# Kernel optimization log

Hardware: AMD Instinct MI355X
Metric: run time of the kernel (lower is better)

The kernel has to match this reference:

```python
import jax, jax.numpy as jnp
import numpy as np

EPS = 1e-6


def setup_inputs() -> dict:
    key = jax.random.key(0)
    k1, k2, k3, k4 = jax.random.split(key, 4)
    B, N, D = 8, 4096, 512
    x = jax.random.normal(k1, (B, N, D), dtype=jnp.float32)
    # torch nn.Linear(dim, 3*dim, bias=False): weight shape [3D, D], y = x @ W.T
    w_qkv = jax.random.normal(k2, (3 * D, D), dtype=jnp.float32) * (1.0 / np.sqrt(D))
    w_proj = jax.random.normal(k3, (D, D), dtype=jnp.float32) * (1.0 / np.sqrt(D))
    b_proj = jax.random.normal(k4, (D,), dtype=jnp.float32) * 0.01
    return {"x": x, "w_qkv": w_qkv, "w_proj": w_proj, "b_proj": b_proj, "heads": 8}


def reference(x, w_qkv, w_proj, b_proj, heads):
    B, N, D = x.shape
    H = heads
    d = D // H
    # qkv projection -> (3, B, H, N, d)
    qkv = (x @ w_qkv.T).reshape(B, N, 3, H, d).transpose(2, 0, 3, 1, 4)
    q, k, v = qkv[0], qkv[1], qkv[2]
    # elu+1 feature map (positive features)
    q = jax.nn.elu(q) + 1.0 + EPS
    k = jax.nn.elu(k) + 1.0 + EPS
    # kv summary: [B,H,d,d]
    kv = jnp.einsum('bhnd,bhne->bhde', k, v)
    # denominator: q . sum_n(k) -> [B,H,N]
    denom = jnp.einsum('bhnd,bhd->bhn', q, k.sum(axis=2))
    out = jnp.einsum('bhnd,bhde->bhne', q, kv) / (denom[..., None] + EPS)
    out = out.transpose(0, 2, 1, 3).reshape(B, N, D)
    return out @ w_proj.T + b_proj
```

## Files before the change

### kernel.cpp

```cpp
#include <hip/hip_runtime.h>
#include <hip/hip_bf16.h>
#include <math.h>

#define EPSF 1e-6f

constexpr int Bc = 8;
constexpr int Nc = 4096;
constexpr int Dc = 512;
constexpr int QKVC = 3 * Dc;

typedef __attribute__((ext_vector_type(8))) short short8v;
typedef __attribute__((ext_vector_type(8))) unsigned short ushort8v;
typedef __attribute__((ext_vector_type(4))) float float4v;

__device__ __forceinline__ unsigned short f2bf(float f) {
    union { float f; unsigned int u; } v; v.f = f;
    unsigned int u = v.u;
    return (unsigned short)((u + 0x7fffu + ((u >> 16) & 1u)) >> 16);
}
__device__ __forceinline__ float bf2f(unsigned short h) {
    union { unsigned int u; float f; } v; v.u = ((unsigned int)h) << 16;
    return v.f;
}

typedef __attribute__((address_space(1))) const void gvoid_t;
typedef __attribute__((address_space(3))) void lvoid_t;
__device__ __forceinline__ void llds16(const void* g, void* l) {
    __builtin_amdgcn_global_load_lds((gvoid_t*)g, (lvoid_t*)l, 16, 0, 0);
}

__global__ __launch_bounds__(256) void cvt_f32_bf16(
    const float* __restrict__ in, unsigned short* __restrict__ out, int n8)
{
    int i = blockIdx.x * 256 + threadIdx.x;
    if (i >= n8) return;
    float4 a = reinterpret_cast<const float4*>(in)[2 * i];
    float4 b = reinterpret_cast<const float4*>(in)[2 * i + 1];
    ushort8v o;
    o[0] = f2bf(a.x); o[1] = f2bf(a.y); o[2] = f2bf(a.z); o[3] = f2bf(a.w);
    o[4] = f2bf(b.x); o[5] = f2bf(b.y); o[6] = f2bf(b.z); o[7] = f2bf(b.w);
    reinterpret_cast<ushort8v*>(out)[i] = o;
}

__global__ __launch_bounds__(512, 2) void gemm_qkv(
    const unsigned short* __restrict__ A,
    const unsigned short* __restrict__ Bm,
    unsigned short* __restrict__ Cout)
{
    constexpr int LDA = 512, LDB = 512, LDC = 1536;
    constexpr int NT = 8;
    __shared__ unsigned short ring[3][24576];

    const int t = threadIdx.x;
    const int orig = blockIdx.x;
    const int wg = (orig & 7) * 192 + (orig >> 3);
    const int bm = (wg / 12) * 256;
    const int bn = (wg % 12) * 128;

    const int w = t >> 6, lane = t & 63;
    const int ln = lane & 15, g = lane >> 4;
    const int wr = (w >> 1) * 64;
    const int wc = (w & 1) * 64;
    const int l7 = ln & 7;

    const int rs = t >> 3;
    const int ci = t & 7;
    const int swz = ci ^ (rs & 7);
    const unsigned short* As0 = A + (size_t)(bm + rs) * LDA + swz * 8;
    const unsigned short* As1 = A + (size_t)(bm + 64 + rs) * LDA + swz * 8;
    const unsigned short* As2 = A + (size_t)(bm + 128 + rs) * LDA + swz * 8;
    const unsigned short* As3 = A + (size_t)(bm + 192 + rs) * LDA + swz * 8;
    const unsigned short* Bs0 = Bm + (size_t)(bn + rs) * LDB + swz * 8;
    const unsigned short* Bs1 = Bm + (size_t)(bn + 64 + rs) * LDB + swz * 8;

#define STAGEQ(Tt) do {                                                        \
        const int k0_ = (Tt) * 64;                                             \
        unsigned short* dA_ = &ring[(Tt) % 3][0];                              \
        unsigned short* dB_ = &ring[(Tt) % 3][16384];                          \
        llds16(As0 + k0_, dA_ + (size_t)t * 8);                                \
        llds16(As1 + k0_, dA_ + (size_t)(512 + t) * 8);                        \
        llds16(As2 + k0_, dA_ + (size_t)(1024 + t) * 8);                       \
        llds16(As3 + k0_, dA_ + (size_t)(1536 + t) * 8);                       \
        llds16(Bs0 + k0_, dB_ + (size_t)t * 8);                                \
        llds16(Bs1 + k0_, dB_ + (size_t)(512 + t) * 8);                        \
    } while (0)

    float4v acc[4][4];
#pragma unroll
    for (int i = 0; i < 4; ++i)
#pragma unroll
        for (int j = 0; j < 4; ++j) acc[i][j] = {0.f, 0.f, 0.f, 0.f};

    STAGEQ(0);
    STAGEQ(1);
    asm volatile("s_waitcnt vmcnt(6)" ::: "memory");
    __builtin_amdgcn_s_barrier();
    __builtin_amdgcn_sched_barrier(0);

#pragma unroll
    for (int T = 0; T < NT; ++T) {
        if (T + 2 < NT) STAGEQ(T + 2);

        const unsigned short* base = &ring[T % 3][0];
        short8v a[4][2], b[4][2];
#pragma unroll
        for (int i = 0; i < 4; ++i)
#pragma unroll
            for (int kk = 0; kk < 2; ++kk) {
                const int row = wr + i * 16 + ln;
                a[i][kk] = *reinterpret_cast<const short8v*>(
                    base + row * 64 + (((kk * 4 + g) ^ l7) << 3));
            }
#pragma unroll
        for (int j = 0; j < 4; ++j)
#pragma unroll
            for (int kk = 0; kk < 2; ++kk) {
                const int row = wc + j * 16 + ln;
                b[j][kk] = *reinterpret_cast<const short8v*>(
                    base + 16384 + row * 64 + (((kk * 4 + g) ^ l7) << 3));
            }

        __builtin_amdgcn_s_setprio(1);
#pragma unroll
        for (int kk = 0; kk < 2; ++kk)
#pragma unroll
            for (int i = 0; i < 4; ++i)
#pragma unroll
                for (int j = 0; j < 4; ++j)
                    acc[i][j] = __builtin_amdgcn_mfma_f32_16x16x32_bf16(
                        a[i][kk], b[j][kk], acc[i][j], 0, 0, 0);
        __builtin_amdgcn_s_setprio(0);

        if (T + 1 < NT) {
            if (T + 2 < NT)
                asm volatile("s_waitcnt vmcnt(6)" ::: "memory");
            else
                asm volatile("s_waitcnt vmcnt(0)" ::: "memory");
            __builtin_amdgcn_s_barrier();
            __builtin_amdgcn_sched_barrier(0);
        }
    }
#undef STAGEQ

#pragma unroll
    for (int i = 0; i < 4; ++i) {
        const int Rb = bm + wr + i * 16 + g * 4;
#pragma unroll
        for (int j = 0; j < 4; ++j) {
            const int Cc = bn + wc + j * 16 + ln;
            const bool do_elu = (Cc < 1024);
#pragma unroll
            for (int r = 0; r < 4; ++r) {
                float v = acc[i][j][r];
                if (do_elu) v = (v > 0.f) ? (v + 1.0f + EPSF) : (expf(v) + EPSF);
                Cout[(size_t)(Rb + r) * LDC + Cc] = f2bf(v);
            }
        }
    }
}

__global__ __launch_bounds__(256) void kv_part(
    const unsigned short* __restrict__ qkv,
    float* __restrict__ kvp, float* __restrict__ ksp)
{
    const int bh = blockIdx.x, chunk = blockIdx.y;
    const int b = bh >> 3, h = bh & 7;

    __shared__ float kt[64][68];
    __shared__ float vt[64][68];
    __shared__ float ksl[4][64];

    const int t  = threadIdx.x;
    const int e  = t & 63, dg = t >> 6;
    const int rr = t >> 3, slot = t & 7;

    float acc[16] = {};
    float ks = 0.f;

    const size_t base = ((size_t)b * Nc + (size_t)chunk * 512) * QKVC + h * 64;

    for (int n0 = 0; n0 < 512; n0 += 64) {
#pragma unroll
        for (int half = 0; half < 2; ++half) {
            const int row = rr + half * 32;
            const unsigned short* kr = qkv + base + (size_t)(n0 + row) * QKVC + Dc + slot * 8;
            const unsigned short* vr = kr + Dc;
            ushort8v kq = *reinterpret_cast<const ushort8v*>(kr);
            ushort8v vq = *reinterpret_cast<const ushort8v*>(vr);
            float4 k0 = make_float4(bf2f(kq[0]), bf2f(kq[1]), bf2f(kq[2]), bf2f(kq[3]));
            float4 k1 = make_float4(bf2f(kq[4]), bf2f(kq[5]), bf2f(kq[6]), bf2f(kq[7]));
            float4 v0 = make_float4(bf2f(vq[0]), bf2f(vq[1]), bf2f(vq[2]), bf2f(vq[3]));
            float4 v1 = make_float4(bf2f(vq[4]), bf2f(vq[5]), bf2f(vq[6]), bf2f(vq[7]));
            *reinterpret_cast<float4*>(&kt[row][slot * 8])     = k0;
            *reinterpret_cast<float4*>(&kt[row][slot * 8 + 4]) = k1;
            *reinterpret_cast<float4*>(&vt[row][slot * 8])     = v0;
            *reinterpret_cast<float4*>(&vt[row][slot * 8 + 4]) = v1;
        }
        __syncthreads();
#pragma unroll 2
        for (int nn = 0; nn < 64; ++nn) {
            const float vv = vt[nn][e];
            const float4 q0 = *reinterpret_cast<const float4*>(&kt[nn][dg * 16]);
            const float4 q1 = *reinterpret_cast<const float4*>(&kt[nn][dg * 16 + 4]);
            const float4 q2 = *reinterpret_cast<const float4*>(&kt[nn][dg * 16 + 8]);
            const float4 q3 = *reinterpret_cast<const float4*>(&kt[nn][dg * 16 + 12]);
            acc[0]  += q0.x * vv; acc[1]  += q0.y * vv; acc[2]  += q0.z * vv; acc[3]  += q0.w * vv;
            acc[4]  += q1.x * vv; acc[5]  += q1.y * vv; acc[6]  += q1.z * vv; acc[7]  += q1.w * vv;
            acc[8]  += q2.x * vv; acc[9]  += q2.y * vv; acc[10] += q2.z * vv; acc[11] += q2.w * vv;
            acc[12] += q3.x * vv; acc[13] += q3.y * vv; acc[14] += q3.z * vv; acc[15] += q3.w * vv;
        }
#pragma unroll
        for (int nn = 0; nn < 16; ++nn) ks += kt[dg * 16 + nn][e];
        __syncthreads();
    }

    float* kvpp = kvp + ((size_t)bh * 8 + chunk) * 4096;
#pragma unroll
    for (int i = 0; i < 16; ++i) kvpp[(dg * 16 + i) * 64 + e] = acc[i];

    ksl[dg][e] = ks;
    __syncthreads();
    if (t < 64) ksp[((size_t)bh * 8 + chunk) * 64 + t] =
        ksl[0][t] + ksl[1][t] + ksl[2][t] + ksl[3][t];
}

__global__ __launch_bounds__(256) void kv_reduce(
    const float* __restrict__ kvp, const float* __restrict__ ksp,
    unsigned short* __restrict__ kvT, float* __restrict__ ksum)
{
    const int bh = blockIdx.x, t = threadIdx.x;
    const float* src = kvp + (size_t)bh * 8 * 4096;
#pragma unroll
    for (int i = 0; i < 16; ++i) {
        const int idx = i * 256 + t;
        float s = 0.f;
#pragma unroll
        for (int c = 0; c < 8; ++c) s += src[c * 4096 + idx];
        const int d = idx >> 6, e = idx & 63;
        kvT[(size_t)bh * 4096 + e * 64 + d] = f2bf(s);
    }
    if (t < 64) {
        float s = 0.f;
#pragma unroll
        for (int c = 0; c < 8; ++c) s += ksp[((size_t)bh * 8 + c) * 64 + t];
        ksum[bh * 64 + t] = s;
    }
}

__global__ __launch_bounds__(256) void attn_proj(
    const unsigned short* __restrict__ qkv,
    const unsigned short* __restrict__ kvT,
    const float* __restrict__ ksum,
    const unsigned short* __restrict__ wp,
    const float* __restrict__ bias,
    float* __restrict__ out)
{
    __shared__ unsigned short lq[128 * 64];
    __shared__ unsigned short lkv[64 * 64];
    __shared__ unsigned short lwp[128 * 64];
    __shared__ unsigned short loL[128 * 64];

    const int t = threadIdx.x;
    const int rowBlk = blockIdx.x;
    const int bn = blockIdx.y;
    const int b = rowBlk >> 5;
    const size_t rowBase = (size_t)rowBlk * 128;

    const int w = t >> 6, lane = t & 63;
    const int ln = lane & 15, g = lane >> 4;
    const int wr = (w >> 1) * 64, wc = (w & 1) * 64;
    const int l7 = ln & 7;

    char* lqc  = (char*)lq;
    char* lkvc = (char*)lkv;
    char* lwpc = (char*)lwp;
    char* loLc = (char*)loL;

    float4v accP[4][4];
#pragma unroll
    for (int i = 0; i < 4; ++i)
#pragma unroll
        for (int j = 0; j < 4; ++j) accP[i][j] = {0.f, 0.f, 0.f, 0.f};

    for (int h = 0; h < 8; ++h) {
        const int bh = b * 8 + h;
        const unsigned short* qsrc = qkv + rowBase * QKVC + h * 64;
        const unsigned short* wsrc = wp + (size_t)(bn * 128) * 512 + h * 64;
        const unsigned short* ksrc = kvT + (size_t)bh * 4096;

#pragma unroll
        for (int s = 0; s < 4; ++s) {
            const int c = s * 256 + t, r = c >> 3, ci = c & 7;
            ushort8v qv = *reinterpret_cast<const ushort8v*>(qsrc + (size_t)r * QKVC + ci * 8);
            *reinterpret_cast<ushort8v*>(lqc + r * 128 + ((ci ^ (r & 7)) << 4)) = qv;
            ushort8v wv = *reinterpret_cast<const ushort8v*>(wsrc + (size_t)r * 512 + ci * 8);
            *reinterpret_cast<ushort8v*>(lwpc + r * 128 + ((ci ^ (r & 7)) << 4)) = wv;
        }
#pragma unroll
        for (int s = 0; s < 2; ++s) {
            const int c = s * 256 + t, r = c >> 3, ci = c & 7;
            ushort8v kvv = *reinterpret_cast<const ushort8v*>(ksrc + r * 64 + ci * 8);
            *reinterpret_cast<ushort8v*>(lkvc + r * 128 + ((ci ^ (r & 7)) << 4)) = kvv;
        }
        __syncthreads();

        float ksv[2][8];
        {
            const float* ksb = ksum + bh * 64 + g * 8;
            float4 a0 = *reinterpret_cast<const float4*>(ksb);
            float4 a1 = *reinterpret_cast<const float4*>(ksb + 4);
            float4 b0 = *reinterpret_cast<const float4*>(ksb + 32);
            float4 b1 = *reinterpret_cast<const float4*>(ksb + 36);
            ksv[0][0] = a0.x; ksv[0][1] = a0.y; ksv[0][2] = a0.z; ksv[0][3] = a0.w;
            ksv[0][4] = a1.x; ksv[0][5] = a1.y; ksv[0][6] = a1.z; ksv[0][7] = a1.w;
            ksv[1][0] = b0.x; ksv[1][1] = b0.y; ksv[1][2] = b0.z; ksv[1][3] = b0.w;
            ksv[1][4] = b1.x; ksv[1][5] = b1.y; ksv[1][6] = b1.z; ksv[1][7] = b1.w;
        }

        short8v akv[4][2], bq[2][2];
#pragma unroll
        for (int i = 0; i < 4; ++i)
#pragma unroll
            for (int kk = 0; kk < 2; ++kk)
                akv[i][kk] = *reinterpret_cast<const short8v*>(
                    lkvc + (i * 16 + ln) * 128 + (((kk * 4 + g) ^ l7) << 4));
#pragma unroll
        for (int j = 0; j < 2; ++j)
#pragma unroll
            for (int kk = 0; kk < 2; ++kk)
                bq[j][kk] = *reinterpret_cast<const short8v*>(
                    lqc + (w * 32 + j * 16 + ln) * 128 + (((kk * 4 + g) ^ l7) << 4));

        float4v acco[4][2];
#pragma unroll
        for (int i = 0; i < 4; ++i)
#pragma unroll
            for (int j = 0; j < 2; ++j) acco[i][j] = {0.f, 0.f, 0.f, 0.f};
#pragma unroll
        for (int kk = 0; kk < 2; ++kk)
#pragma unroll
            for (int i = 0; i < 4; ++i)
#pragma unroll
                for (int j = 0; j < 2; ++j)
                    acco[i][j] = __builtin_amdgcn_mfma_f32_16x16x32_bf16(
                        akv[i][kk], bq[j][kk], acco[i][j], 0, 0, 0);

        float inv[2];
#pragma unroll
        for (int j = 0; j < 2; ++j) {
            float p = 0.f;
#pragma unroll
            for (int kk = 0; kk < 2; ++kk)
#pragma unroll
                for (int m = 0; m < 8; ++m)
                    p += bf2f((unsigned short)bq[j][kk][m]) * ksv[kk][m];
            p += __shfl_xor(p, 16);
            p += __shfl_xor(p, 32);
            inv[j] = 1.0f / (p + EPSF);
        }

#pragma unroll
        for (int i = 0; i < 4; ++i)
#pragma unroll
            for (int j = 0; j < 2; ++j) {
                unsigned int p0 = (unsigned int)f2bf(acco[i][j][0] * inv[j]) |
                                  ((unsigned int)f2bf(acco[i][j][1] * inv[j]) << 16);
                unsigned int p1 = (unsigned int)f2bf(acco[i][j][2] * inv[j]) |
                                  ((unsigned int)f2bf(acco[i][j][3] * inv[j]) << 16);
                const int row = w * 32 + j * 16 + ln;
                const int chunk = i * 2 + (g >> 1);
                char* dst = loLc + row * 128 + (((chunk ^ l7) << 4) | ((g & 1) << 3));
                *reinterpret_cast<uint2*>(dst) = make_uint2(p0, p1);
            }
        __syncthreads();

        short8v ao[4][2], bw[4][2];
#pragma unroll
        for (int i = 0; i < 4; ++i)
#pragma unroll
            for (int kk = 0; kk < 2; ++kk)
                ao[i][kk] = *reinterpret_cast<const short8v*>(
                    loLc + (wr + i * 16 + ln) * 128 + (((kk * 4 + g) ^ l7) << 4));
#pragma unroll
        for (int j = 0; j < 4; ++j)
#pragma unroll
            for (int kk = 0; kk < 2; ++kk)
                bw[j][kk] = *reinterpret_cast<const short8v*>(
                    lwpc + (wc + j * 16 + ln) * 128 + (((kk * 4 + g) ^ l7) << 4));

        __builtin_amdgcn_s_setprio(1);
#pragma unroll
        for (int kk = 0; kk < 2; ++kk)
#pragma unroll
            for (int i = 0; i < 4; ++i)
#pragma unroll
                for (int j = 0; j < 4; ++j)
                    accP[i][j] = __builtin_amdgcn_mfma_f32_16x16x32_bf16(
                        ao[i][kk], bw[j][kk], accP[i][j], 0, 0, 0);
        __builtin_amdgcn_s_setprio(0);
        __syncthreads();
    }

#pragma unroll
    for (int j = 0; j < 4; ++j) {
        const int col = bn * 128 + wc + j * 16 + ln;
        const float bv = bias[col];
#pragma unroll
        for (int i = 0; i < 4; ++i) {
            const size_t rg = rowBase + wr + i * 16 + g * 4;
#pragma unroll
            for (int rr = 0; rr < 4; ++rr)
                out[(rg + rr) * 512 + col] = accP[i][j][rr] + bv;
        }
    }
}

extern "C" void kernel_launch(void* const* d_in, const int* in_sizes, int n_in,
                              void* d_out, int out_size, void* d_ws, size_t ws_size,
                              hipStream_t stream)
{
    const float* x      = (const float*)d_in[0];
    const float* w_qkv  = (const float*)d_in[1];
    const float* w_proj = (const float*)d_in[2];
    const float* b_proj = (const float*)d_in[3];
    float* out = (float*)d_out;

    char* ws = (char*)d_ws;
    unsigned short* qkvb = (unsigned short*)ws;
    size_t off = (size_t)32768 * 1536 * 2;
    unsigned short* xb   = (unsigned short*)(ws + off); off += (size_t)32768 * 512 * 2;
    unsigned short* wqb  = (unsigned short*)(ws + off); off += (size_t)1536 * 512 * 2;
    unsigned short* wpb  = (unsigned short*)(ws + off); off += (size_t)512 * 512 * 2;
    float* kvp           = (float*)(ws + off);          off += (size_t)64 * 8 * 4096 * 4;
    float* ksp           = (float*)(ws + off);          off += (size_t)64 * 8 * 64 * 4;
    unsigned short* kvT  = (unsigned short*)(ws + off); off += (size_t)64 * 4096 * 2;
    float* ksumb         = (float*)(ws + off);

    cvt_f32_bf16<<<dim3((32768 * 512 / 8 + 255) / 256), dim3(256), 0, stream>>>(x, xb, 32768 * 512 / 8);
    cvt_f32_bf16<<<dim3((1536 * 512 / 8 + 255) / 256), dim3(256), 0, stream>>>(w_qkv, wqb, 1536 * 512 / 8);
    cvt_f32_bf16<<<dim3((512 * 512 / 8 + 255) / 256), dim3(256), 0, stream>>>(w_proj, wpb, 512 * 512 / 8);

    gemm_qkv<<<dim3(1536), dim3(512), 0, stream>>>(xb, wqb, qkvb);

    kv_part<<<dim3(64, 8), dim3(256), 0, stream>>>(qkvb, kvp, ksp);
    kv_reduce<<<dim3(64), dim3(256), 0, stream>>>(kvp, ksp, kvT, ksumb);

    attn_proj<<<dim3(256, 4), dim3(256), 0, stream>>>(
        qkvb, kvT, ksumb, wpb, b_proj, out);
}
```

Before: 195.2 us.

## Use 256x256 QKV GEMM tiles with double buffering and interleaved phased staging

The QKV GEMM tile grows from 256x128 to 256x256, halving the grid to 768 blocks, and each wave now covers a 128x64 sub-tile. The 3-stage LDS ring becomes a double buffer, with loads for the next k-tile split into four chunks that are issued between barrier-separated MFMA phases. The aim is more data reuse per LDS byte and global loads that overlap compute in a ping-pong schedule. In exchange it uses 64KB of LDS and twice the accumulator registers, which may lower occupancy below the 2 blocks requested, and it adds more barriers per k-step.

Measured after the change: 203.3 us. 4.2% more time.

```diff
diff --git a/kernel.cpp b/kernel.cpp
--- a/kernel.cpp
+++ b/kernel.cpp
@@ -49,109 +49,130 @@
 {
     constexpr int LDA = 512, LDB = 512, LDC = 1536;
     constexpr int NT = 8;
-    __shared__ unsigned short ring[3][24576];
+    __shared__ unsigned short lA[2][16384];
+    __shared__ unsigned short lB[2][16384];
 
     const int t = threadIdx.x;
     const int orig = blockIdx.x;
-    const int wg = (orig & 7) * 192 + (orig >> 3);
-    const int bm = (wg / 12) * 256;
-    const int bn = (wg % 12) * 128;
+    const int wg = (orig & 7) * 96 + (orig >> 3);
+    const int bm = (wg / 6) * 256;
+    const int bn = (wg % 6) * 256;
 
     const int w = t >> 6, lane = t & 63;
     const int ln = lane & 15, g = lane >> 4;
-    const int wr = (w >> 1) * 64;
-    const int wc = (w & 1) * 64;
+    const int wm = (w >> 2) * 128;
+    const int wn = (w & 3) * 64;
     const int l7 = ln & 7;
 
-    const int rs = t >> 3;
-    const int ci = t & 7;
+    const int rs = t >> 3, ci = t & 7;
     const int swz = ci ^ (rs & 7);
-    const unsigned short* As0 = A + (size_t)(bm + rs) * LDA + swz * 8;
-    const unsigned short* As1 = A + (size_t)(bm + 64 + rs) * LDA + swz * 8;
-    const unsigned short* As2 = A + (size_t)(bm + 128 + rs) * LDA + swz * 8;
-    const unsigned short* As3 = A + (size_t)(bm + 192 + rs) * LDA + swz * 8;
-    const unsigned short* Bs0 = Bm + (size_t)(bn + rs) * LDB + swz * 8;
-    const unsigned short* Bs1 = Bm + (size_t)(bn + 64 + rs) * LDB + swz * 8;
-
-#define STAGEQ(Tt) do {                                                        \
-        const int k0_ = (Tt) * 64;                                             \
-        unsigned short* dA_ = &ring[(Tt) % 3][0];                              \
-        unsigned short* dB_ = &ring[(Tt) % 3][16384];                          \
-        llds16(As0 + k0_, dA_ + (size_t)t * 8);                                \
-        llds16(As1 + k0_, dA_ + (size_t)(512 + t) * 8);                        \
-        llds16(As2 + k0_, dA_ + (size_t)(1024 + t) * 8);                       \
-        llds16(As3 + k0_, dA_ + (size_t)(1536 + t) * 8);                       \
-        llds16(Bs0 + k0_, dB_ + (size_t)t * 8);                                \
-        llds16(Bs1 + k0_, dB_ + (size_t)(512 + t) * 8);                        \
-    } while (0)
-
-    float4v acc[4][4];
-#pragma unroll
-    for (int i = 0; i < 4; ++i)
+    const unsigned short* Ab = A + (size_t)(bm + rs) * LDA + swz * 8;
+    const unsigned short* Bb = Bm + (size_t)(bn + rs) * LDB + swz * 8;
+
+#define STG_A(Tt, r4) llds16(Ab + (size_t)(r4) * 64 * LDA + (Tt) * 64, \
+                             &lA[(Tt) & 1][((r4) * 512 + t) * 8])
+#define STG_B(Tt, r4) llds16(Bb + (size_t)(r4) * 64 * LDB + (Tt) * 64, \
+                             &lB[(Tt) & 1][((r4) * 512 + t) * 8])
+#define PH_BAR() do { __builtin_amdgcn_s_barrier(); \
+                      __builtin_amdgcn_sched_barrier(0); } while (0)
+
+    float4v acc[8][4];
+#pragma unroll
+    for (int i = 0; i < 8; ++i)
 #pragma unroll
         for (int j = 0; j < 4; ++j) acc[i][j] = {0.f, 0.f, 0.f, 0.f};
 
-    STAGEQ(0);
-    STAGEQ(1);
-    asm volatile("s_waitcnt vmcnt(6)" ::: "memory");
-    __builtin_amdgcn_s_barrier();
-    __builtin_amdgcn_sched_barrier(0);
+    STG_A(0, 0); STG_A(0, 1); STG_A(0, 2); STG_A(0, 3);
+    STG_B(0, 0); STG_B(0, 1); STG_B(0, 2); STG_B(0, 3);
+    asm volatile("s_waitcnt vmcnt(0)" ::: "memory");
+    PH_BAR();
 
 #pragma unroll
     for (int T = 0; T < NT; ++T) {
-        if (T + 2 < NT) STAGEQ(T + 2);
-
-        const unsigned short* base = &ring[T % 3][0];
-        short8v a[4][2], b[4][2];
-#pragma unroll
-        for (int i = 0; i < 4; ++i)
-#pragma unroll
-            for (int kk = 0; kk < 2; ++kk) {
-                const int row = wr + i * 16 + ln;
-                a[i][kk] = *reinterpret_cast<const short8v*>(
-                    base + row * 64 + (((kk * 4 + g) ^ l7) << 3));
-            }
-#pragma unroll
-        for (int j = 0; j < 4; ++j)
-#pragma unroll
-            for (int kk = 0; kk < 2; ++kk) {
-                const int row = wc + j * 16 + ln;
-                b[j][kk] = *reinterpret_cast<const short8v*>(
-                    base + 16384 + row * 64 + (((kk * 4 + g) ^ l7) << 3));
-            }
-
+        const unsigned short* pa = lA[T & 1];
+        const unsigned short* pb = lB[T & 1];
+        const bool st = (T + 1 < NT);
+        short8v a[4], b[4];
+
+#define RDA(mf, kk) (*reinterpret_cast<const short8v*>( \
+            pa + (wm + (mf) * 16 + ln) * 64 + (((((kk) << 2) + g) ^ l7) << 3)))
+#define RDB(nf, kk) (*reinterpret_cast<const short8v*>( \
+            pb + (wn + (nf) * 16 + ln) * 64 + (((((kk) << 2) + g) ^ l7) << 3)))
+
+#pragma unroll
+        for (int nf = 0; nf < 4; ++nf) b[nf] = RDB(nf, 0);
+#pragma unroll
+        for (int i = 0; i < 4; ++i) a[i] = RDA(i, 0);
+        if (st) { STG_A(T + 1, 0); STG_A(T + 1, 1); }
+        PH_BAR();
         __builtin_amdgcn_s_setprio(1);
 #pragma unroll
-        for (int kk = 0; kk < 2; ++kk)
-#pragma unroll
-            for (int i = 0; i < 4; ++i)
-#pragma unroll
-                for (int j = 0; j < 4; ++j)
-                    acc[i][j] = __builtin_amdgcn_mfma_f32_16x16x32_bf16(
-                        a[i][kk], b[j][kk], acc[i][j], 0, 0, 0);
+        for (int i = 0; i < 4; ++i)
+#pragma unroll
+            for (int nf = 0; nf < 4; ++nf)
+                acc[i][nf] = __builtin_amdgcn_mfma_f32_16x16x32_bf16(a[i], b[nf], acc[i][nf], 0, 0, 0);
         __builtin_amdgcn_s_setprio(0);
-
-        if (T + 1 < NT) {
-            if (T + 2 < NT)
-                asm volatile("s_waitcnt vmcnt(6)" ::: "memory");
-            else
-                asm volatile("s_waitcnt vmcnt(0)" ::: "memory");
-            __builtin_amdgcn_s_barrier();
-            __builtin_amdgcn_sched_barrier(0);
-        }
-    }
-#undef STAGEQ
-
-#pragma unroll
-    for (int i = 0; i < 4; ++i) {
-        const int Rb = bm + wr + i * 16 + g * 4;
-#pragma unroll
-        for (int j = 0; j < 4; ++j) {
-            const int Cc = bn + wc + j * 16 + ln;
+        PH_BAR();
+
+#pragma unroll
+        for (int i = 0; i < 4; ++i) a[i] = RDA(4 + i, 0);
+        if (st) { STG_A(T + 1, 2); STG_A(T + 1, 3); }
+        PH_BAR();
+        __builtin_amdgcn_s_setprio(1);
+#pragma unroll
+        for (int i = 0; i < 4; ++i)
+#pragma unroll
+            for (int nf = 0; nf < 4; ++nf)
+                acc[4 + i][nf] = __builtin_amdgcn_mfma_f32_16x16x32_bf16(a[i], b[nf], acc[4 + i][nf], 0, 0, 0);
+        __builtin_amdgcn_s_setprio(0);
+        PH_BAR();
+
+#pragma unroll
+        for (int nf = 0; nf < 4; ++nf) b[nf] = RDB(nf, 1);
+#pragma unroll
+        for (int i = 0; i < 4; ++i) a[i] = RDA(i, 1);
+        if (st) { STG_B(T + 1, 0); STG_B(T + 1, 1); }
+        PH_BAR();
+        __builtin_amdgcn_s_setprio(1);
+#pragma unroll
+        for (int i = 0; i < 4; ++i)
+#pragma unroll
+            for (int nf = 0; nf < 4; ++nf)
+                acc[i][nf] = __builtin_amdgcn_mfma_f32_16x16x32_bf16(a[i], b[nf], acc[i][nf], 0, 0, 0);
+        __builtin_amdgcn_s_setprio(0);
+        PH_BAR();
+
+#pragma unroll
+        for (int i = 0; i < 4; ++i) a[i] = RDA(4 + i, 1);
+        if (st) { STG_B(T + 1, 2); STG_B(T + 1, 3); }
+        PH_BAR();
+        __builtin_amdgcn_s_setprio(1);
+#pragma unroll
+        for (int i = 0; i < 4; ++i)
+#pragma unroll
+            for (int nf = 0; nf < 4; ++nf)
+                acc[4 + i][nf] = __builtin_amdgcn_mfma_f32_16x16x32_bf16(a[i], b[nf], acc[4 + i][nf], 0, 0, 0);
+        __builtin_amdgcn_s_setprio(0);
+        if (st) asm volatile("s_waitcnt vmcnt(0)" ::: "memory");
+        PH_BAR();
+
+#undef RDA
+#undef RDB
+    }
+#undef STG_A
+#undef STG_B
+#undef PH_BAR
+
+#pragma unroll
+    for (int mf = 0; mf < 8; ++mf) {
+        const int Rb = bm + wm + mf * 16 + g * 4;
+#pragma unroll
+        for (int nf = 0; nf < 4; ++nf) {
+            const int Cc = bn + wn + nf * 16 + ln;
             const bool do_elu = (Cc < 1024);
 #pragma unroll
             for (int r = 0; r < 4; ++r) {
-                float v = acc[i][j][r];
+                float v = acc[mf][nf][r];
                 if (do_elu) v = (v > 0.f) ? (v + 1.0f + EPSF) : (expf(v) + EPSF);
                 Cout[(size_t)(Rb + r) * LDC + Cc] = f2bf(v);
             }
@@ -440,7 +461,7 @@
     cvt_f32_bf16<<<dim3((1536 * 512 / 8 + 255) / 256), dim3(256), 0, stream>>>(w_qkv, wqb, 1536 * 512 / 8);
     cvt_f32_bf16<<<dim3((512 * 512 / 8 + 255) / 256), dim3(256), 0, stream>>>(w_proj, wpb, 512 * 512 / 8);
 
-    gemm_qkv<<<dim3(1536), dim3(512), 0, stream>>>(xb, wqb, qkvb);
+    gemm_qkv<<<dim3(768), dim3(512), 0, stream>>>(xb, wqb, qkvb);
 
     kv_part<<<dim3(64, 8), dim3(256), 0, stream>>>(qkvb, kvp, ksp);
     kv_reduce<<<dim3(64), dim3(256), 0, stream>>>(kvp, ksp, kvT, ksumb);
```

## Fold kv summary into output projection weights and run a single pipelined GEMM

Applied to the files above, without the earlier changes.

Precomputes per-batch matrices M = kv·W_projᵀ for each head, so the output becomes (q/denom)·M + bias. That turns the per-head two-stage attn_proj into one K=512 GEMM with a triple-buffered LDS ring, plus a small q_scale pass that normalises q in place. The aim is to drop the intermediate per-head kv multiply and its LDS round-trip. In exchange it adds two launches, a read-modify-write of q, and an extra bf16 rounding of q/denom and of M.

Result: no change. 192.5 us (-1.4%).

```diff
diff --git a/kernel.cpp b/kernel.cpp
--- a/kernel.cpp
+++ b/kernel.cpp
@@ -226,7 +226,7 @@
 
 __global__ __launch_bounds__(256) void kv_reduce(
     const float* __restrict__ kvp, const float* __restrict__ ksp,
-    unsigned short* __restrict__ kvT, float* __restrict__ ksum)
+    unsigned short* __restrict__ kvb, float* __restrict__ ksum)
 {
     const int bh = blockIdx.x, t = threadIdx.x;
     const float* src = kvp + (size_t)bh * 8 * 4096;
@@ -236,8 +236,7 @@
         float s = 0.f;
 #pragma unroll
         for (int c = 0; c < 8; ++c) s += src[c * 4096 + idx];
-        const int d = idx >> 6, e = idx & 63;
-        kvT[(size_t)bh * 4096 + e * 64 + d] = f2bf(s);
+        kvb[(size_t)bh * 4096 + idx] = f2bf(s);
     }
     if (t < 64) {
         float s = 0.f;
@@ -247,170 +246,200 @@
     }
 }
 
-__global__ __launch_bounds__(256) void attn_proj(
-    const unsigned short* __restrict__ qkv,
-    const unsigned short* __restrict__ kvT,
-    const float* __restrict__ ksum,
+__global__ __launch_bounds__(256) void gemm_M(
+    const unsigned short* __restrict__ kvb,
     const unsigned short* __restrict__ wp,
+    unsigned short* __restrict__ MT)
+{
+    const int bh = blockIdx.x, b = bh >> 3, h = bh & 7;
+    const int t = threadIdx.x, w = t >> 6, lane = t & 63;
+    const int ln = lane & 15, g = lane >> 4;
+
+    float4v acc[8][4];
+#pragma unroll
+    for (int i = 0; i < 8; ++i)
+#pragma unroll
+        for (int j = 0; j < 4; ++j) acc[i][j] = {0.f, 0.f, 0.f, 0.f};
+
+#pragma unroll
+    for (int kk = 0; kk < 2; ++kk) {
+        short8v a[8], bf[4];
+#pragma unroll
+        for (int i = 0; i < 8; ++i)
+            a[i] = *reinterpret_cast<const short8v*>(
+                wp + (size_t)(w * 128 + i * 16 + ln) * 512 + h * 64 + kk * 32 + g * 8);
+#pragma unroll
+        for (int j = 0; j < 4; ++j)
+            bf[j] = *reinterpret_cast<const short8v*>(
+                kvb + (size_t)bh * 4096 + (j * 16 + ln) * 64 + kk * 32 + g * 8);
+#pragma unroll
+        for (int i = 0; i < 8; ++i)
+#pragma unroll
+            for (int j = 0; j < 4; ++j)
+                acc[i][j] = __builtin_amdgcn_mfma_f32_16x16x32_bf16(a[i], bf[j], acc[i][j], 0, 0, 0);
+    }
+
+#pragma unroll
+    for (int i = 0; i < 8; ++i) {
+        const int c0 = w * 128 + i * 16 + g * 4;
+#pragma unroll
+        for (int j = 0; j < 4; ++j) {
+            const int d = j * 16 + ln;
+#pragma unroll
+            for (int r = 0; r < 4; ++r)
+                MT[(size_t)b * 262144 + (size_t)(c0 + r) * 512 + h * 64 + d] =
+                    f2bf(acc[i][j][r]);
+        }
+    }
+}
+
+__global__ __launch_bounds__(256) void q_scale(
+    unsigned short* __restrict__ qkv, const float* __restrict__ ksum)
+{
+    __shared__ float kss[512];
+    const int blk = blockIdx.x;
+    const int b = blk >> 7;
+    const int t = threadIdx.x;
+    kss[t] = ksum[b * 512 + t];
+    kss[t + 256] = ksum[b * 512 + 256 + t];
+    __syncthreads();
+
+    const int row = blk * 32 + (t >> 3);
+    const int h = t & 7;
+    unsigned short* p = qkv + (size_t)row * QKVC + h * 64;
+
+    ushort8v v[8];
+#pragma unroll
+    for (int s = 0; s < 8; ++s) v[s] = *reinterpret_cast<const ushort8v*>(p + s * 8);
+
+    float den = EPSF;
+#pragma unroll
+    for (int s = 0; s < 8; ++s)
+#pragma unroll
+        for (int m = 0; m < 8; ++m)
+            den += bf2f(v[s][m]) * kss[h * 64 + s * 8 + m];
+    const float inv = 1.0f / den;
+
+#pragma unroll
+    for (int s = 0; s < 8; ++s) {
+        ushort8v o;
+#pragma unroll
+        for (int m = 0; m < 8; ++m) o[m] = f2bf(bf2f(v[s][m]) * inv);
+        *reinterpret_cast<ushort8v*>(p + s * 8) = o;
+    }
+}
+
+__global__ __launch_bounds__(512, 2) void gemm_out(
+    const unsigned short* __restrict__ A,
+    const unsigned short* __restrict__ Bt,
     const float* __restrict__ bias,
     float* __restrict__ out)
 {
-    __shared__ unsigned short lq[128 * 64];
-    __shared__ unsigned short lkv[64 * 64];
-    __shared__ unsigned short lwp[128 * 64];
-    __shared__ unsigned short loL[128 * 64];
+    constexpr int LDA = 1536, LDB = 512, NT = 8;
+    __shared__ unsigned short ring[3][24576];
 
     const int t = threadIdx.x;
-    const int rowBlk = blockIdx.x;
-    const int bn = blockIdx.y;
-    const int b = rowBlk >> 5;
-    const size_t rowBase = (size_t)rowBlk * 128;
+    const int orig = blockIdx.x;
+    const int wg = (orig & 7) * 64 + (orig >> 3);
+    const int bm = (wg >> 2) * 256;
+    const int bn = (wg & 3) * 128;
+    const unsigned short* Bm = Bt + (size_t)(bm >> 12) * 262144;
 
     const int w = t >> 6, lane = t & 63;
     const int ln = lane & 15, g = lane >> 4;
-    const int wr = (w >> 1) * 64, wc = (w & 1) * 64;
+    const int wr = (w >> 1) * 64;
+    const int wc = (w & 1) * 64;
     const int l7 = ln & 7;
 
-    char* lqc  = (char*)lq;
-    char* lkvc = (char*)lkv;
-    char* lwpc = (char*)lwp;
-    char* loLc = (char*)loL;
-
-    float4v accP[4][4];
+    const int rs = t >> 3;
+    const int ci = t & 7;
+    const int swz = ci ^ (rs & 7);
+    const unsigned short* As0 = A + (size_t)(bm + rs) * LDA + swz * 8;
+    const unsigned short* As1 = A + (size_t)(bm + 64 + rs) * LDA + swz * 8;
+    const unsigned short* As2 = A + (size_t)(bm + 128 + rs) * LDA + swz * 8;
+    const unsigned short* As3 = A + (size_t)(bm + 192 + rs) * LDA + swz * 8;
+    const unsigned short* Bs0 = Bm + (size_t)(bn + rs) * LDB + swz * 8;
+    const unsigned short* Bs1 = Bm + (size_t)(bn + 64 + rs) * LDB + swz * 8;
+
+#define STAGEO(Tt) do {                                                        \
+        const int k0_ = (Tt) * 64;                                             \
+        unsigned short* dA_ = &ring[(Tt) % 3][0];                              \
+        unsigned short* dB_ = &ring[(Tt) % 3][16384];                          \
+        llds16(As0 + k0_, dA_ + (size_t)t * 8);                                \
+        llds16(As1 + k0_, dA_ + (size_t)(512 + t) * 8);                        \
+        llds16(As2 + k0_, dA_ + (size_t)(1024 + t) * 8);                       \
+        llds16(As3 + k0_, dA_ + (size_t)(1536 + t) * 8);                       \
+        llds16(Bs0 + k0_, dB_ + (size_t)t * 8);                                \
+        llds16(Bs1 + k0_, dB_ + (size_t)(512 + t) * 8);                        \
+    } while (0)
+
+    float4v acc[4][4];
 #pragma unroll
     for (int i = 0; i < 4; ++i)
 #pragma unroll
-        for (int j = 0; j < 4; ++j) accP[i][j] = {0.f, 0.f, 0.f, 0.f};
-
-    for (int h = 0; h < 8; ++h) {
-        const int bh = b * 8 + h;
-        const unsigned short* qsrc = qkv + rowBase * QKVC + h * 64;
-        const unsigned short* wsrc = wp + (size_t)(bn * 128) * 512 + h * 64;
-        const unsigned short* ksrc = kvT + (size_t)bh * 4096;
-
-#pragma unroll
-        for (int s = 0; s < 4; ++s) {
-            const int c = s * 256 + t, r = c >> 3, ci = c & 7;
-            ushort8v qv = *reinterpret_cast<const ushort8v*>(qsrc + (size_t)r * QKVC + ci * 8);
-            *reinterpret_cast<ushort8v*>(lqc + r * 128 + ((ci ^ (r & 7)) << 4)) = qv;
-            ushort8v wv = *reinterpret_cast<const ushort8v*>(wsrc + (size_t)r * 512 + ci * 8);
-            *reinterpret_cast<ushort8v*>(lwpc + r * 128 + ((ci ^ (r & 7)) << 4)) = wv;
-        }
-#pragma unroll
-        for (int s = 0; s < 2; ++s) {
-            const int c = s * 256 + t, r = c >> 3, ci = c & 7;
-            ushort8v kvv = *reinterpret_cast<const ushort8v*>(ksrc + r * 64 + ci * 8);
-            *reinterpret_cast<ushort8v*>(lkvc + r * 128 + ((ci ^ (r & 7)) << 4)) = kvv;
-        }
-        __syncthreads();
-
-        float ksv[2][8];
-        {
-            const float* ksb = ksum + bh * 64 + g * 8;
-            float4 a0 = *reinterpret_cast<const float4*>(ksb);
-            float4 a1 = *reinterpret_cast<const float4*>(ksb + 4);
-            float4 b0 = *reinterpret_cast<const float4*>(ksb + 32);
-            float4 b1 = *reinterpret_cast<const float4*>(ksb + 36);
-            ksv[0][0] = a0.x; ksv[0][1] = a0.y; ksv[0][2] = a0.z; ksv[0][3] = a0.w;
-            ksv[0][4] = a1.x; ksv[0][5] = a1.y; ksv[0][6] = a1.z; ksv[0][7] = a1.w;
-            ksv[1][0] = b0.x; ksv[1][1] = b0.y; ksv[1][2] = b0.z; ksv[1][3] = b0.w;
-            ksv[1][4] = b1.x; ksv[1][5] = b1.y; ksv[1][6] = b1.z; ksv[1][7] = b1.w;
-        }
-
-        short8v akv[4][2], bq[2][2];
+        for (int j = 0; j < 4; ++j) acc[i][j] = {0.f, 0.f, 0.f, 0.f};
+
+    STAGEO(0);
+    STAGEO(1);
+    asm volatile("s_waitcnt vmcnt(6)" ::: "memory");
+    __builtin_amdgcn_s_barrier();
+    __builtin_amdgcn_sched_barrier(0);
+
+#pragma unroll
+    for (int T = 0; T < NT; ++T) {
+        if (T + 2 < NT) STAGEO(T + 2);
+
+        const unsigned short* base = &ring[T % 3][0];
+        short8v a[4][2], b[4][2];
 #pragma unroll
         for (int i = 0; i < 4; ++i)
 #pragma unroll
-            for (int kk = 0; kk < 2; ++kk)
-                akv[i][kk] = *reinterpret_cast<const short8v*>(
-                    lkvc + (i * 16 + ln) * 128 + (((kk * 4 + g) ^ l7) << 4));
-#pragma unroll
-        for (int j = 0; j < 2; ++j)
-#pragma unroll
-            for (int kk = 0; kk < 2; ++kk)
-                bq[j][kk] = *reinterpret_cast<const short8v*>(
-                    lqc + (w * 32 + j * 16 + ln) * 128 + (((kk * 4 + g) ^ l7) << 4));
-
-        float4v acco[4][2];
-#pragma unroll
-        for (int i = 0; i < 4; ++i)
-#pragma unroll
-            for (int j = 0; j < 2; ++j) acco[i][j] = {0.f, 0.f, 0.f, 0.f};
+            for (int kk = 0; kk < 2; ++kk) {
+                const int row = wr + i * 16 + ln;
+                a[i][kk] = *reinterpret_cast<const short8v*>(
+                    base + row * 64 + (((kk * 4 + g) ^ l7) << 3));
+            }
+#pragma unroll
+        for (int j = 0; j < 4; ++j)
+#pragma unroll
+            for (int kk = 0; kk < 2; ++kk) {
+                const int row = wc + j * 16 + ln;
+                b[j][kk] = *reinterpret_cast<const short8v*>(
+                    base + 16384 + row * 64 + (((kk * 4 + g) ^ l7) << 3));
+            }
+
+        __builtin_amdgcn_s_setprio(1);
 #pragma unroll
         for (int kk = 0; kk < 2; ++kk)
 #pragma unroll
             for (int i = 0; i < 4; ++i)
 #pragma unroll
-                for (int j = 0; j < 2; ++j)
-                    acco[i][j] = __builtin_amdgcn_mfma_f32_16x16x32_bf16(
-                        akv[i][kk], bq[j][kk], acco[i][j], 0, 0, 0);
-
-        float inv[2];
-#pragma unroll
-        for (int j = 0; j < 2; ++j) {
-            float p = 0.f;
-#pragma unroll
-            for (int kk = 0; kk < 2; ++kk)
-#pragma unroll
-                for (int m = 0; m < 8; ++m)
-                    p += bf2f((unsigned short)bq[j][kk][m]) * ksv[kk][m];
-            p += __shfl_xor(p, 16);
-            p += __shfl_xor(p, 32);
-            inv[j] = 1.0f / (p + EPSF);
-        }
-
-#pragma unroll
-        for (int i = 0; i < 4; ++i)
-#pragma unroll
-            for (int j = 0; j < 2; ++j) {
-                unsigned int p0 = (unsigned int)f2bf(acco[i][j][0] * inv[j]) |
-                                  ((unsigned int)f2bf(acco[i][j][1] * inv[j]) << 16);
-                unsigned int p1 = (unsigned int)f2bf(acco[i][j][2] * inv[j]) |
-                                  ((unsigned int)f2bf(acco[i][j][3] * inv[j]) << 16);
-                const int row = w * 32 + j * 16 + ln;
-                const int chunk = i * 2 + (g >> 1);
-                char* dst = loLc + row * 128 + (((chunk ^ l7) << 4) | ((g & 1) << 3));
-                *reinterpret_cast<uint2*>(dst) = make_uint2(p0, p1);
-            }
-        __syncthreads();
-
-        short8v ao[4][2], bw[4][2];
-#pragma unroll
-        for (int i = 0; i < 4; ++i)
-#pragma unroll
-            for (int kk = 0; kk < 2; ++kk)
-                ao[i][kk] = *reinterpret_cast<const short8v*>(
-                    loLc + (wr + i * 16 + ln) * 128 + (((kk * 4 + g) ^ l7) << 4));
-#pragma unroll
-        for (int j = 0; j < 4; ++j)
-#pragma unroll
-            for (int kk = 0; kk < 2; ++kk)
-                bw[j][kk] = *reinterpret_cast<const short8v*>(
-                    lwpc + (wc + j * 16 + ln) * 128 + (((kk * 4 + g) ^ l7) << 4));
-
-        __builtin_amdgcn_s_setprio(1);
-#pragma unroll
-        for (int kk = 0; kk < 2; ++kk)
-#pragma unroll
-            for (int i = 0; i < 4; ++i)
-#pragma unroll
                 for (int j = 0; j < 4; ++j)
-                    accP[i][j] = __builtin_amdgcn_mfma_f32_16x16x32_bf16(
-                        ao[i][kk], bw[j][kk], accP[i][j], 0, 0, 0);
+                    acc[i][j] = __builtin_amdgcn_mfma_f32_16x16x32_bf16(
+                        a[i][kk], b[j][kk], acc[i][j], 0, 0, 0);
         __builtin_amdgcn_s_setprio(0);
-        __syncthreads();
-    }
-
-#pragma unroll
-    for (int j = 0; j < 4; ++j) {
-        const int col = bn * 128 + wc + j * 16 + ln;
-        const float bv = bias[col];
-#pragma unroll
-        for (int i = 0; i < 4; ++i) {
-            const size_t rg = rowBase + wr + i * 16 + g * 4;
-#pragma unroll
-            for (int rr = 0; rr < 4; ++rr)
-                out[(rg + rr) * 512 + col] = accP[i][j][rr] + bv;
+
+        if (T + 1 < NT) {
+            if (T + 2 < NT)
+                asm volatile("s_waitcnt vmcnt(6)" ::: "memory");
+            else
+                asm volatile("s_waitcnt vmcnt(0)" ::: "memory");
+            __builtin_amdgcn_s_barrier();
+            __builtin_amdgcn_sched_barrier(0);
+        }
+    }
+#undef STAGEO
+
+#pragma unroll
+    for (int i = 0; i < 4; ++i) {
+        const int Rb = bm + wr + i * 16 + g * 4;
+#pragma unroll
+        for (int j = 0; j < 4; ++j) {
+            const int Cc = bn + wc + j * 16 + ln;
+            const float bv = bias[Cc];
+#pragma unroll
+            for (int r = 0; r < 4; ++r)
+                out[(size_t)(Rb + r) * 512 + Cc] = acc[i][j][r] + bv;
         }
     }
 }
@@ -433,8 +462,9 @@
     unsigned short* wpb  = (unsigned short*)(ws + off); off += (size_t)512 * 512 * 2;
     float* kvp           = (float*)(ws + off);          off += (size_t)64 * 8 * 4096 * 4;
     float* ksp           = (float*)(ws + off);          off += (size_t)64 * 8 * 64 * 4;
-    unsigned short* kvT  = (unsigned short*)(ws + off); off += (size_t)64 * 4096 * 2;
-    float* ksumb         = (float*)(ws + off);
+    unsigned short* kvb  = (unsigned short*)(ws + off); off += (size_t)64 * 4096 * 2;
+    float* ksumb         = (float*)(ws + off);          off += (size_t)64 * 64 * 4;
+    unsigned short* MT   = (unsigned short*)(ws + off); off += (size_t)8 * 512 * 512 * 2;
 
     cvt_f32_bf16<<<dim3((32768 * 512 / 8 + 255) / 256), dim3(256), 0, stream>>>(x, xb, 32768 * 512 / 8);
     cvt_f32_bf16<<<dim3((1536 * 512 / 8 + 255) / 256), dim3(256), 0, stream>>>(w_qkv, wqb, 1536 * 512 / 8);
@@ -443,8 +473,11 @@
     gemm_qkv<<<dim3(1536), dim3(512), 0, stream>>>(xb, wqb, qkvb);
 
     kv_part<<<dim3(64, 8), dim3(256), 0, stream>>>(qkvb, kvp, ksp);
-    kv_reduce<<<dim3(64), dim3(256), 0, stream>>>(kvp, ksp, kvT, ksumb);
-
-    attn_proj<<<dim3(256, 4), dim3(256), 0, stream>>>(
-        qkvb, kvT, ksumb, wpb, b_proj, out);
-}
+    kv_reduce<<<dim3(64), dim3(256), 0, stream>>>(kvp, ksp, kvb, ksumb);
+
+    gemm_M<<<dim3(64), dim3(256), 0, stream>>>(kvb, wpb, MT);
+
+    q_scale<<<dim3(1024), dim3(256), 0, stream>>>(qkvb, ksumb);
+
+    gemm_out<<<dim3(512), dim3(512), 0, stream>>>(qkvb, MT, b_proj, out);
+}
```
